# Kernel optimization log

Hardware: AMD Instinct MI355X
Metric: run time of the kernel (lower is better)

The kernel has to match this reference:

```python
import jax, jax.numpy as jnp
import numpy as np

TWO_PI = 2.0 * np.pi
OMEGA = 1.0  # frequency scale from init


def setup_inputs() -> dict:
    key = jax.random.key(0)
    ks = jax.random.split(key, 10)
    B, G, D = 2, 32, 3
    C_IN, C, C_OUT, F, L = 4, 128, 2, 128, 4  # in/model/out channels, freqs, n_spectral_convs
    a = jax.random.normal(ks[0], (B, G, G, G, C_IN), dtype=jnp.float32)
    x = jax.random.uniform(ks[1], (B, G, G, G, D), dtype=jnp.float32)
    y = jax.random.uniform(ks[2], (B, G, G, G, D), dtype=jnp.float32)
    fc_in_w = jax.random.normal(ks[3], (C_IN, C), dtype=jnp.float32) / np.sqrt(C_IN)
    fc_in_b = jnp.zeros((C,), dtype=jnp.float32)
    freqs = jax.random.normal(ks[4], (L, F, D), dtype=jnp.float32)  # per-layer spatial frequencies
    w_real = jax.random.normal(ks[5], (L, C, C, F), dtype=jnp.float32) * 0.05
    w_imag = jax.random.normal(ks[6], (L, C, C, F), dtype=jnp.float32) * 0.05
    fc_out_w = jax.random.normal(ks[7], (C, C_OUT), dtype=jnp.float32) / np.sqrt(C)
    fc_out_b = jnp.zeros((C_OUT,), dtype=jnp.float32)
    return {"a": a, "x": x, "y": y, "fc_in_w": fc_in_w, "fc_in_b": fc_in_b,
            "freqs": freqs, "w_real": w_real, "w_imag": w_imag,
            "fc_out_w": fc_out_w, "fc_out_b": fc_out_b}


def _spectral_conv(hf, xin, xout, k, Wc):
    # hf: (B, N, C) real; xin/xout: (B, N, D); k: (F, D); Wc: (C, C, F) complex
    N = hf.shape[1]
    ang_in = TWO_PI * OMEGA * jnp.einsum('bnd,fd->bnf', xin, k)
    phi_in = jnp.exp(-1j * ang_in.astype(jnp.complex64))          # (B, N, F)
    H = jnp.einsum('bnc,bnf->bcf', hf.astype(jnp.complex64), phi_in) / N  # forward transform
    G = jnp.einsum('bcf,cof->bof', H, Wc)                          # per-frequency channel mixing
    ang_out = TWO_PI * OMEGA * jnp.einsum('bnd,fd->bnf', xout, k)
    phi_out = jnp.exp(1j * ang_out.astype(jnp.complex64))          # (B, N, F)
    return jnp.real(jnp.einsum('bof,bnf->bno', G, phi_out))       # inverse evaluation at xout


def reference(a, x, y, fc_in_w, fc_in_b, freqs, w_real, w_imag, fc_out_w, fc_out_b):
    B = a.shape[0]
    spatial = a.shape[1:4]
    hf = jnp.einsum('...i,io->...o', a, fc_in_w) + fc_in_b
    hf = hf.reshape(B, -1, hf.shape[-1])               # (B, N, C)
    xf = x.reshape(B, -1, x.shape[-1])                 # (B, N, D)
    yf = y.reshape(B, -1, y.shape[-1])
    L = freqs.shape[0]
    for l in range(L):
        Wc = (w_real[l] + 1j * w_imag[l]).astype(jnp.complex64)
        pts_out = xf if l < L - 1 else yf              # last conv queries at y
        hf = jax.nn.gelu(_spectral_conv(hf, xf, pts_out, freqs[l], Wc))
    u = jnp.einsum('bnc,co->bno', hf, fc_out_w) + fc_out_b
    return u.reshape(B, *spatial, fc_out_w.shape[-1])
```

## Files before the change

### kernel.cpp

```cpp
#include <hip/hip_runtime.h>
#include <math.h>

#define Bb 2
#define Nn 32768
#define Cc 128
#define Ff 128
#define LL 4
#define SKN 128
#define PS 16448

typedef __attribute__((ext_vector_type(8))) short short8;
typedef __attribute__((ext_vector_type(4))) float float4v;
typedef __attribute__((ext_vector_type(2))) unsigned int uint2v;
typedef unsigned short ushort_t;
typedef unsigned int uint_t;

union frag_cast { short8 s; uint_t u[4]; };
union vec8 { float4v v[2]; float s[8]; };

__device__ inline uint_t asu(float f) { union { float f; uint_t u; } x; x.f = f; return x.u; }
__device__ inline float asf(uint_t u) { union { uint_t u; float f; } x; x.u = u; return x.f; }
__device__ inline uint_t pack_hi(float v0, float v1) {
    return __builtin_amdgcn_perm(asu(v1), asu(v0), 0x07060302u);
}
__device__ inline float resid(float v) { return v - asf(asu(v) & 0xffff0000u); }

typedef __attribute__((address_space(1))) const uint_t guint;
typedef __attribute__((address_space(3))) uint_t luint;
__device__ inline void gload16(const uint_t* g, uint_t* l) {
    __builtin_amdgcn_global_load_lds((guint*)g, (luint*)l, 16, 0, 0);
}

#define LBAR() asm volatile("s_waitcnt lgkmcnt(0)\n\ts_barrier" ::: "memory")
#define CBAR() asm volatile("s_waitcnt vmcnt(6) lgkmcnt(0)\n\ts_barrier" ::: "memory")

__global__ __launch_bounds__(256) void prep_xt(const float* __restrict__ x,
                                               const float* __restrict__ y,
                                               float* __restrict__ xT,
                                               float* __restrict__ yT) {
    int i = blockIdx.x * 256 + threadIdx.x;
    int b = i >> 15, n = i & 32767;
    const float* xp = x + (size_t)i * 3;
    const float* yp = y + (size_t)i * 3;
    size_t base = ((size_t)(b * 3) << 15) + n;
    xT[base] = xp[0]; xT[base + (1 << 15)] = xp[1]; xT[base + (2 << 15)] = xp[2];
    yT[base] = yp[0]; yT[base + (1 << 15)] = yp[1]; yT[base + (2 << 15)] = yp[2];
}

__global__ __launch_bounds__(256) void in_proj(const float* __restrict__ a,
                                               const float* __restrict__ w,
                                               const float* __restrict__ bias,
                                               uint_t* __restrict__ hfTh,
                                               uint_t* __restrict__ hfTl) {
    int idx = blockIdx.x * 256 + threadIdx.x;
    int np = idx & 16383;
    int c = (idx >> 14) & 127;
    int b = idx >> 21;
    int n = np * 2;
    const float* ap = a + (((size_t)(b << 15)) + n) * 4;
    float s0 = bias[c], s1 = s0;
#pragma unroll
    for (int i = 0; i < 4; ++i) { s0 += ap[i] * w[i * Cc + c]; s1 += ap[4 + i] * w[i * Cc + c]; }
    hfTh[idx] = pack_hi(s0, s1);
    hfTl[idx] = pack_hi(resid(s0), resid(s1));
}

__global__ __launch_bounds__(512, 2) void fwd_lds(const uint_t* __restrict__ hfTh,
                                                  const uint_t* __restrict__ hfTl,
                                                  const float* __restrict__ xT,
                                                  const float* __restrict__ freqs,
                                                  float* __restrict__ Spart) {
    __shared__ __align__(16) uint_t Ah_s[2][2048], Al_s[2][2048];

    const int sk = blockIdx.x;
    const int b = blockIdx.y;
    const int tid = threadIdx.x, lane = tid & 63, wave = tid >> 6;
    const int h = wave & 1, wn = wave >> 1;
    const int fr = lane & 15, kg = lane >> 4;

    float kx[2], ky[2], kz[2];
#pragma unroll
    for (int ni = 0; ni < 2; ++ni) {
        int f = wn * 32 + ni * 16 + fr;
        kx[ni] = freqs[f * 3 + 0];
        ky[ni] = freqs[f * 3 + 1];
        kz[ni] = freqs[f * 3 + 2];
    }

    const float* xb = xT + ((size_t)(b * 3) << 15);

    const int srow = wave * 16 + (lane >> 2);
    const size_t gbase = ((size_t)(b * 128 + srow) << 14) + (size_t)((lane & 3) * 4);
    const int npair0 = sk * 128;

    float4v acc[8][2];
#pragma unroll
    for (int mi = 0; mi < 8; ++mi)
#pragma unroll
        for (int ni = 0; ni < 2; ++ni) acc[mi][ni] = (float4v){0.f, 0.f, 0.f, 0.f};

    vec8 X0[2], X1[2], X2[2];
    gload16(hfTh + gbase + npair0, &Ah_s[0][wave * 256]);
    gload16(hfTl + gbase + npair0, &Al_s[0][wave * 256]);
    __builtin_amdgcn_sched_barrier(0);
    {
        const int nbase = sk * 256 + kg * 8;
        X0[0].v[0] = *(const float4v*)(xb + nbase);
        X0[0].v[1] = *(const float4v*)(xb + nbase + 4);
        X1[0].v[0] = *(const float4v*)(xb + (1 << 15) + nbase);
        X1[0].v[1] = *(const float4v*)(xb + (1 << 15) + nbase + 4);
        X2[0].v[0] = *(const float4v*)(xb + (2 << 15) + nbase);
        X2[0].v[1] = *(const float4v*)(xb + (2 << 15) + nbase + 4);
    }

#pragma unroll
    for (int kt = 0; kt < 8; ++kt) {
        const int cur = kt & 1, nxt = cur ^ 1;
        CBAR();
        if (kt < 7) {
            gload16(hfTh + gbase + npair0 + (kt + 1) * 16, &Ah_s[nxt][wave * 256]);
            gload16(hfTl + gbase + npair0 + (kt + 1) * 16, &Al_s[nxt][wave * 256]);
            __builtin_amdgcn_sched_barrier(0);
            const int nbase2 = sk * 256 + (kt + 1) * 32 + kg * 8;
            X0[nxt].v[0] = *(const float4v*)(xb + nbase2);
            X0[nxt].v[1] = *(const float4v*)(xb + nbase2 + 4);
            X1[nxt].v[0] = *(const float4v*)(xb + (1 << 15) + nbase2);
            X1[nxt].v[1] = *(const float4v*)(xb + (1 << 15) + nbase2 + 4);
            X2[nxt].v[0] = *(const float4v*)(xb + (2 << 15) + nbase2);
            X2[nxt].v[1] = *(const float4v*)(xb + (2 << 15) + nbase2 + 4);
        }
        float r[16], tv[16];
#pragma unroll
        for (int ni = 0; ni < 2; ++ni)
#pragma unroll
            for (int q = 0; q < 4; ++q) {
                float rv0 = X0[cur].s[2 * q] * kx[ni] + X1[cur].s[2 * q] * ky[ni] + X2[cur].s[2 * q] * kz[ni];
                float rv1 = X0[cur].s[2 * q + 1] * kx[ni] + X1[cur].s[2 * q + 1] * ky[ni] + X2[cur].s[2 * q + 1] * kz[ni];
                r[ni * 8 + 2 * q] = __builtin_amdgcn_fractf(rv0);
                r[ni * 8 + 2 * q + 1] = __builtin_amdgcn_fractf(rv1);
            }
        if (h) {
#pragma unroll
            for (int i = 0; i < 16; ++i) tv[i] = __builtin_amdgcn_sinf(r[i]);
        } else {
#pragma unroll
            for (int i = 0; i < 16; ++i) tv[i] = __builtin_amdgcn_cosf(r[i]);
        }
        frag_cast bhf[2], blf[2];
#pragma unroll
        for (int ni = 0; ni < 2; ++ni)
#pragma unroll
            for (int q = 0; q < 4; ++q) {
                float v0 = tv[ni * 8 + 2 * q], v1 = tv[ni * 8 + 2 * q + 1];
                bhf[ni].u[q] = pack_hi(v0, v1);
                blf[ni].u[q] = pack_hi(resid(v0), resid(v1));
            }
#pragma unroll
        for (int mi = 0; mi < 8; ++mi) {
            frag_cast ah, al;
            ah.s = *(const short8*)&Ah_s[cur][(mi * 16 + fr) * 16 + kg * 4];
            al.s = *(const short8*)&Al_s[cur][(mi * 16 + fr) * 16 + kg * 4];
#pragma unroll
            for (int ni = 0; ni < 2; ++ni) {
                acc[mi][ni] = __builtin_amdgcn_mfma_f32_16x16x32_bf16(ah.s, bhf[ni].s, acc[mi][ni], 0, 0, 0);
                acc[mi][ni] = __builtin_amdgcn_mfma_f32_16x16x32_bf16(ah.s, blf[ni].s, acc[mi][ni], 0, 0, 0);
                acc[mi][ni] = __builtin_amdgcn_mfma_f32_16x16x32_bf16(al.s, bhf[ni].s, acc[mi][ni], 0, 0, 0);
            }
        }
    }

    float* op = Spart + (size_t)((b * 2 + h) * SKN + sk) * PS;
#pragma unroll
    for (int mi = 0; mi < 8; ++mi)
#pragma unroll
        for (int ni = 0; ni < 2; ++ni)
#pragma unroll
            for (int r2 = 0; r2 < 4; ++r2) {
                int c = mi * 16 + kg * 4 + r2;
                int f = wn * 32 + ni * 16 + fr;
                op[c * 128 + f] = acc[mi][ni][r2];
            }
}

__global__ __launch_bounds__(256) void reduce_kernel(const float* __restrict__ Spart,
                                                     float* __restrict__ S) {
    __shared__ float red[4][64];
    const int chunk = blockIdx.x, bh = blockIdx.y;
    const int tid = threadIdx.x;
    const int cfl = tid & 63, q = tid >> 6;
    const float* p = Spart + (size_t)bh * SKN * PS + (size_t)(q * 32) * PS + chunk * 64 + cfl;
    float s = 0.0f;
#pragma unroll 8
    for (int k = 0; k < 32; ++k) s += p[(size_t)k * PS];
    red[q][cfl] = s;
    __syncthreads();
    if (tid < 64) {
        float t = red[0][tid] + red[1][tid] + red[2][tid] + red[3][tid];
        S[bh * 16384 + chunk * 64 + tid] = t;
    }
}

__global__ __launch_bounds__(256) void mix_kernel(const float* __restrict__ S,
                                                  const float* __restrict__ Wre,
                                                  const float* __restrict__ Wim,
                                                  uint_t* __restrict__ Gh,
                                                  uint_t* __restrict__ Gl) {
    __shared__ float Stile[4][128][16];
    const int ot = blockIdx.x;
    const int ft = blockIdx.y;
    const int tid = threadIdx.x;
    const int fl = tid & 15, ol = (tid >> 4) & 1, cg = tid >> 5;
    const int o = ot * 2 + ol, f0 = ft * 16;

    for (int i = tid; i < 8192; i += 256) {
        int bh = i >> 11, c = (i >> 4) & 127, ff = i & 15;
        Stile[bh][c][ff] = S[(size_t)bh * 16384 + c * 128 + f0 + ff];
    }
    __syncthreads();

    float g0 = 0.f, g1 = 0.f, g2 = 0.f, g3 = 0.f;
#pragma unroll 4
    for (int c = cg * 16; c < cg * 16 + 16; ++c) {
        float wr = Wre[((size_t)(c * 128 + o)) * 128 + f0 + fl];
        float wi = Wim[((size_t)(c * 128 + o)) * 128 + f0 + fl];
        float sc0 = Stile[0][c][fl], ss0 = Stile[1][c][fl];
        float sc1 = Stile[2][c][fl], ss1 = Stile[3][c][fl];
        g0 += sc0 * wr + ss0 * wi;  g1 += ss0 * wr - sc0 * wi;
        g2 += sc1 * wr + ss1 * wi;  g3 += ss1 * wr - sc1 * wi;
    }
    __syncthreads();
    float4v* rp = (float4v*)Stile;
    rp[cg * 32 + ol * 16 + fl] = (float4v){g0, g1, g2, g3};
    __syncthreads();
    if (tid < 32) {
        int tol = tid >> 4, tfl = tid & 15;
        float4v r = rp[tid];
#pragma unroll
        for (int j = 1; j < 8; ++j) r += rp[j * 32 + tid];
        const float invN = 1.0f / (float)Nn;
        float gre0 = r[0] * invN, gmi0 = r[1] * invN;
        float gre1 = r[2] * invN, gmi1 = r[3] * invN;
        int oo = ot * 2 + tol;
        Gh[(0 * 128 + oo) * 128 + f0 + tfl] = pack_hi(gre0, gmi0);
        Gl[(0 * 128 + oo) * 128 + f0 + tfl] = pack_hi(resid(gre0), resid(gmi0));
        Gh[(1 * 128 + oo) * 128 + f0 + tfl] = pack_hi(gre1, gmi1);
        Gl[(1 * 128 + oo) * 128 + f0 + tfl] = pack_hi(resid(gre1), resid(gmi1));
    }
}

template <int LAST>
__global__ __launch_bounds__(512, 4) void inv_reg(const uint_t* __restrict__ Gh,
                                                  const uint_t* __restrict__ Gl,
                                                  const float* __restrict__ ptsT,
                                                  const float* __restrict__ freqs,
                                                  uint_t* __restrict__ hfTh,
                                                  uint_t* __restrict__ hfTl,
                                                  const float* __restrict__ ow,
                                                  const float* __restrict__ ob,
                                                  float* __restrict__ u) {
    __shared__ __align__(16) float kxs[128], kys[128], kzs[128];
    __shared__ __align__(16) uint_t Ah_s[4096];
    __shared__ __align__(16) uint_t Al_s[4096];
    __shared__ float redo[8][32][2];
    const int nt = blockIdx.x, b = blockIdx.y;
    const int tid = threadIdx.x, lane = tid & 63, wn = tid >> 6;
    const int fr = lane & 15, kg = lane >> 4;

    if (tid < 128) {
        kxs[tid] = freqs[tid * 3 + 0];
        kys[tid] = freqs[tid * 3 + 1];
        kzs[tid] = freqs[tid * 3 + 2];
    }

    frag_cast bh[8], bl[8];
#pragma unroll
    for (int kt = 0; kt < 8; ++kt) {
        size_t gi = ((size_t)(b * 128 + wn * 16 + fr)) * 128 + kt * 16 + kg * 4;
        bh[kt].s = *(const short8*)(Gh + gi);
        bl[kt].s = *(const short8*)(Gl + gi);
    }

    float w0v = 0.f, w1v = 0.f;
    if (LAST) {
        int o = wn * 16 + fr;
        w0v = ow[o * 2 + 0];
        w1v = ow[o * 2 + 1];
    }

    const float* pb = ptsT + ((size_t)(b * 3) << 15);
    const int n0 = nt * 64;

    float px[4], py[4], pz[4];
#pragma unroll
    for (int m = 0; m < 4; ++m) {
        int n = n0 + m * 16 + fr;
        px[m] = pb[n]; py[m] = pb[(1 << 15) + n]; pz[m] = pb[(2 << 15) + n];
    }

    __syncthreads();

#pragma unroll
    for (int ph = 0; ph < 2; ++ph) {
        {
            const int kt = wn;
            float4v kxv = *(const float4v*)&kxs[kt * 16 + kg * 4];
            float4v kyv = *(const float4v*)&kys[kt * 16 + kg * 4];
            float4v kzv = *(const float4v*)&kzs[kt * 16 + kg * 4];
#pragma unroll
            for (int mi2 = 0; mi2 < 2; ++mi2) {
                const int m = ph * 2 + mi2;
                frag_cast ah, al;
#pragma unroll
                for (int q = 0; q < 4; ++q) {
                    float rev = px[m] * kxv[q] + py[m] * kyv[q] + pz[m] * kzv[q];
                    float rr = __builtin_amdgcn_fractf(rev);
                    float cv = __builtin_amdgcn_cosf(rr);
                    float sv = __builtin_amdgcn_sinf(rr);
                    ah.u[q] = pack_hi(cv, sv);
                    al.u[q] = pack_hi(resid(cv), resid(sv));
                }
                *(short8*)&Ah_s[((mi2 * 8 + kt) * 64 + lane) * 4] = ah.s;
                *(short8*)&Al_s[((mi2 * 8 + kt) * 64 + lane) * 4] = al.s;
            }
        }
        LBAR();

        float4v acc[2];
#pragma unroll
        for (int mi2 = 0; mi2 < 2; ++mi2) acc[mi2] = (float4v){0.f, 0.f, 0.f, 0.f};

#pragma unroll
        for (int kt = 0; kt < 8; ++kt) {
#pragma unroll
            for (int mi2 = 0; mi2 < 2; ++mi2) {
                frag_cast ah, al;
                ah.s = *(const short8*)&Ah_s[((mi2 * 8 + kt) * 64 + lane) * 4];
                al.s = *(const short8*)&Al_s[((mi2 * 8 + kt) * 64 + lane) * 4];
                acc[mi2] = __builtin_amdgcn_mfma_f32_16x16x32_bf16(ah.s, bh[kt].s, acc[mi2], 0, 0, 0);
                acc[mi2] = __builtin_amdgcn_mfma_f32_16x16x32_bf16(ah.s, bl[kt].s, acc[mi2], 0, 0, 0);
                acc[mi2] = __builtin_amdgcn_mfma_f32_16x16x32_bf16(al.s, bh[kt].s, acc[mi2], 0, 0, 0);
            }
        }
        LBAR();

        float ps[2][2][4];
        if (LAST) {
#pragma unroll
            for (int mi2 = 0; mi2 < 2; ++mi2)
#pragma unroll
                for (int j = 0; j < 2; ++j)
#pragma unroll
                    for (int r2 = 0; r2 < 4; ++r2) ps[mi2][j][r2] = 0.f;
        }
#pragma unroll
        for (int mi2 = 0; mi2 < 2; ++mi2) {
            const int m = ph * 2 + mi2;
            float g[4];
#pragma unroll
            for (int r2 = 0; r2 < 4; ++r2) {
                float v = acc[mi2][r2];
                float u2 = 1.5957691216057308f * (v + 0.044715f * v * v * v);
                float t = 1.0f - 2.0f / (1.0f + __expf(u2));
                g[r2] = 0.5f * v * (1.0f + t);
            }
            if (!LAST) {
                int o = wn * 16 + fr;
                int nb = n0 + m * 16 + kg * 4;
                size_t di = ((size_t)(b * 128 + o) << 14) + (nb >> 1);
                uint2v hv = { pack_hi(g[0], g[1]), pack_hi(g[2], g[3]) };
                uint2v lv = { pack_hi(resid(g[0]), resid(g[1])), pack_hi(resid(g[2]), resid(g[3])) };
                *(uint2v*)(hfTh + di) = hv;
                *(uint2v*)(hfTl + di) = lv;
            } else {
#pragma unroll
                for (int r2 = 0; r2 < 4; ++r2) {
                    ps[mi2][0][r2] += g[r2] * w0v;
                    ps[mi2][1][r2] += g[r2] * w1v;
                }
            }
        }

        if (LAST) {
#pragma unroll
            for (int mi2 = 0; mi2 < 2; ++mi2)
#pragma unroll
                for (int j = 0; j < 2; ++j)
#pragma unroll
                    for (int r2 = 0; r2 < 4; ++r2) {
                        float v = ps[mi2][j][r2];
                        v += __shfl_xor(v, 1);
                        v += __shfl_xor(v, 2);
                        v += __shfl_xor(v, 4);
                        v += __shfl_xor(v, 8);
                        ps[mi2][j][r2] = v;
                    }
            if (fr == 0) {
#pragma unroll
                for (int mi2 = 0; mi2 < 2; ++mi2)
#pragma unroll
                    for (int r2 = 0; r2 < 4; ++r2) {
                        redo[wn][mi2 * 16 + kg * 4 + r2][0] = ps[mi2][0][r2];
                        redo[wn][mi2 * 16 + kg * 4 + r2][1] = ps[mi2][1][r2];
                    }
            }
            LBAR();
            if (tid < 64) {
                int nl = tid >> 1, j = tid & 1;
                float val = ob[j];
#pragma unroll
                for (int w8 = 0; w8 < 8; ++w8) val += redo[w8][nl][j];
                u[((size_t)((b << 15) + n0 + ph * 32 + nl)) * 2 + j] = val;
            }
            LBAR();
        }
    }
}

extern "C" void kernel_launch(void* const* d_in, const int* in_sizes, int n_in,
                              void* d_out, int out_size, void* d_ws, size_t ws_size,
                              hipStream_t stream) {
    const float* a        = (const float*)d_in[0];
    const float* x        = (const float*)d_in[1];
    const float* y        = (const float*)d_in[2];
    const float* fc_in_w  = (const float*)d_in[3];
    const float* fc_in_b  = (const float*)d_in[4];
    const float* freqs    = (const float*)d_in[5];
    const float* w_real   = (const float*)d_in[6];
    const float* w_imag   = (const float*)d_in[7];
    const float* fc_out_w = (const float*)d_in[8];
    const float* fc_out_b = (const float*)d_in[9];
    float* out = (float*)d_out;

    uint_t* ws    = (uint_t*)d_ws;
    uint_t* hfTh  = ws;
    uint_t* hfTl  = hfTh + (size_t)Bb * Cc * Nn / 2;
    float*  Spart = (float*)(hfTl + (size_t)Bb * Cc * Nn / 2);
    float*  S     = Spart + (size_t)Bb * 2 * SKN * PS;
    uint_t* Gh    = (uint_t*)(S + (size_t)Bb * 2 * Cc * Ff);
    uint_t* Gl    = Gh + (size_t)Bb * Cc * Ff;
    float*  xT    = (float*)(Gl + (size_t)Bb * Cc * Ff);
    float*  yT    = xT + (size_t)Bb * 3 * Nn;

    prep_xt<<<(Bb * Nn) / 256, 256, 0, stream>>>(x, y, xT, yT);
    in_proj<<<(Bb * Cc * Nn / 2) / 256, 256, 0, stream>>>(a, fc_in_w, fc_in_b, hfTh, hfTl);

    for (int l = 0; l < LL; ++l) {
        const float* k   = freqs  + (size_t)l * Ff * 3;
        const float* Wre = w_real + (size_t)l * Cc * Cc * Ff;
        const float* Wim = w_imag + (size_t)l * Cc * Cc * Ff;
        const float* pT  = (l < LL - 1) ? xT : yT;

        fwd_lds<<<dim3(SKN, Bb), 512, 0, stream>>>(hfTh, hfTl, xT, k, Spart);
        reduce_kernel<<<dim3(256, 4), 256, 0, stream>>>(Spart, S);
        mix_kernel<<<dim3(64, 8), 256, 0, stream>>>(S, Wre, Wim, Gh, Gl);
        if (l < LL - 1) {
            inv_reg<0><<<dim3(512, Bb), 512, 0, stream>>>(Gh, Gl, pT, k, hfTh, hfTl,
                                                          nullptr, nullptr, nullptr);
        } else {
            inv_reg<1><<<dim3(512, Bb), 512, 0, stream>>>(Gh, Gl, pT, k, hfTh, hfTl,
                                                          fc_out_w, fc_out_b, out);
        }
    }
}
```

Baseline: 365.9 us.

## Fuse inverse evaluation, GELU and next layer's forward transform into one kernel

Adds an inv_fwd kernel that, per chunk of 256 points, evaluates the inverse transform from the mixed spectrum, applies GELU, and immediately accumulates the next layer's forward transform partial sums from LDS. The hidden activations hfTh/hfTl are no longer written to and re-read from global memory between layers, and one kernel launch per layer is removed. In exchange the fused kernel runs with a larger LDS footprint and register pressure (launch bound 512 threads, 2 blocks) and only 128x2 blocks, which may lower occupancy and parallelism compared with the separate kernels.

```diff
diff --git a/kernel.cpp b/kernel.cpp
--- a/kernel.cpp
+++ b/kernel.cpp
@@ -88,7 +88,6 @@
     }
 
     const float* xb = xT + ((size_t)(b * 3) << 15);
-
     const int srow = wave * 16 + (lane >> 2);
     const size_t gbase = ((size_t)(b * 128 + srow) << 14) + (size_t)((lane & 3) * 4);
     const int npair0 = sk * 128;
@@ -179,6 +178,184 @@
                 int c = mi * 16 + kg * 4 + r2;
                 int f = wn * 32 + ni * 16 + fr;
                 op[c * 128 + f] = acc[mi][ni][r2];
+            }
+}
+
+__global__ __launch_bounds__(512, 2) void inv_fwd(const uint_t* __restrict__ Gh,
+                                                  const uint_t* __restrict__ Gl,
+                                                  const float* __restrict__ xT,
+                                                  const float* __restrict__ fI,
+                                                  const float* __restrict__ fF,
+                                                  float* __restrict__ Spart) {
+    __shared__ float kxs[128], kys[128], kzs[128];
+    __shared__ __align__(16) float Xs[3][256];
+    __shared__ __align__(16) uint_t Ah_s[4096], Al_s[4096];
+    __shared__ __align__(16) uint_t Hh_s[2560], Hl_s[2560];
+    const int chunk = blockIdx.x, b = blockIdx.y;
+    const int tid = threadIdx.x, lane = tid & 63, wn = tid >> 6;
+    const int fr = lane & 15, kg = lane >> 4;
+    const int h = wn & 1, wf = wn >> 1;
+    const int n0 = chunk * 256;
+
+    if (tid < 128) {
+        kxs[tid] = fI[tid * 3 + 0];
+        kys[tid] = fI[tid * 3 + 1];
+        kzs[tid] = fI[tid * 3 + 2];
+    }
+    for (int i = tid; i < 768; i += 512) {
+        int d = i >> 8, nn = i & 255;
+        Xs[d][nn] = xT[((size_t)(b * 3 + d) << 15) + n0 + nn];
+    }
+
+    frag_cast bh[8], bl[8];
+#pragma unroll
+    for (int kt = 0; kt < 8; ++kt) {
+        size_t gi = ((size_t)(b * 128 + wn * 16 + fr)) * 128 + kt * 16 + kg * 4;
+        bh[kt].s = *(const short8*)(Gh + gi);
+        bl[kt].s = *(const short8*)(Gl + gi);
+    }
+
+    float kxf[2], kyf[2], kzf[2];
+#pragma unroll
+    for (int ni = 0; ni < 2; ++ni) {
+        int f = wf * 32 + ni * 16 + fr;
+        kxf[ni] = fF[f * 3 + 0];
+        kyf[ni] = fF[f * 3 + 1];
+        kzf[ni] = fF[f * 3 + 2];
+    }
+
+    float4v accF[8][2];
+#pragma unroll
+    for (int mi = 0; mi < 8; ++mi)
+#pragma unroll
+        for (int ni = 0; ni < 2; ++ni) accF[mi][ni] = (float4v){0.f, 0.f, 0.f, 0.f};
+
+    __syncthreads();
+
+    for (int p = 0; p < 8; ++p) {
+        const int nsub = p * 32;
+
+        {
+            const int kt = wn;
+            float4v kxv = *(const float4v*)&kxs[kt * 16 + kg * 4];
+            float4v kyv = *(const float4v*)&kys[kt * 16 + kg * 4];
+            float4v kzv = *(const float4v*)&kzs[kt * 16 + kg * 4];
+#pragma unroll
+            for (int mi2 = 0; mi2 < 2; ++mi2) {
+                float px = Xs[0][nsub + mi2 * 16 + fr];
+                float py = Xs[1][nsub + mi2 * 16 + fr];
+                float pz = Xs[2][nsub + mi2 * 16 + fr];
+                frag_cast ah, al;
+#pragma unroll
+                for (int q = 0; q < 4; ++q) {
+                    float rev = px * kxv[q] + py * kyv[q] + pz * kzv[q];
+                    float rr = __builtin_amdgcn_fractf(rev);
+                    float cv = __builtin_amdgcn_cosf(rr);
+                    float sv = __builtin_amdgcn_sinf(rr);
+                    ah.u[q] = pack_hi(cv, sv);
+                    al.u[q] = pack_hi(resid(cv), resid(sv));
+                }
+                *(short8*)&Ah_s[((mi2 * 8 + kt) * 64 + lane) * 4] = ah.s;
+                *(short8*)&Al_s[((mi2 * 8 + kt) * 64 + lane) * 4] = al.s;
+            }
+        }
+        LBAR();
+
+        {
+            float4v acc[2];
+#pragma unroll
+            for (int mi2 = 0; mi2 < 2; ++mi2) acc[mi2] = (float4v){0.f, 0.f, 0.f, 0.f};
+#pragma unroll
+            for (int kt = 0; kt < 8; ++kt) {
+#pragma unroll
+                for (int mi2 = 0; mi2 < 2; ++mi2) {
+                    frag_cast ah, al;
+                    ah.s = *(const short8*)&Ah_s[((mi2 * 8 + kt) * 64 + lane) * 4];
+                    al.s = *(const short8*)&Al_s[((mi2 * 8 + kt) * 64 + lane) * 4];
+                    acc[mi2] = __builtin_amdgcn_mfma_f32_16x16x32_bf16(ah.s, bh[kt].s, acc[mi2], 0, 0, 0);
+                    acc[mi2] = __builtin_amdgcn_mfma_f32_16x16x32_bf16(ah.s, bl[kt].s, acc[mi2], 0, 0, 0);
+                    acc[mi2] = __builtin_amdgcn_mfma_f32_16x16x32_bf16(al.s, bh[kt].s, acc[mi2], 0, 0, 0);
+                }
+            }
+#pragma unroll
+            for (int mi2 = 0; mi2 < 2; ++mi2) {
+                float g[4];
+#pragma unroll
+                for (int r2 = 0; r2 < 4; ++r2) {
+                    float v = acc[mi2][r2];
+                    float u2 = 1.5957691216057308f * (v + 0.044715f * v * v * v);
+                    float t = 1.0f - 2.0f / (1.0f + __expf(u2));
+                    g[r2] = 0.5f * v * (1.0f + t);
+                }
+                int row = wn * 16 + fr;
+                uint2v hv = { pack_hi(g[0], g[1]), pack_hi(g[2], g[3]) };
+                uint2v lv = { pack_hi(resid(g[0]), resid(g[1])), pack_hi(resid(g[2]), resid(g[3])) };
+                *(uint2v*)&Hh_s[row * 20 + mi2 * 8 + kg * 2] = hv;
+                *(uint2v*)&Hl_s[row * 20 + mi2 * 8 + kg * 2] = lv;
+            }
+        }
+        LBAR();
+
+        {
+            vec8 x0, x1, x2;
+            x0.v[0] = *(const float4v*)&Xs[0][nsub + kg * 8];
+            x0.v[1] = *(const float4v*)&Xs[0][nsub + kg * 8 + 4];
+            x1.v[0] = *(const float4v*)&Xs[1][nsub + kg * 8];
+            x1.v[1] = *(const float4v*)&Xs[1][nsub + kg * 8 + 4];
+            x2.v[0] = *(const float4v*)&Xs[2][nsub + kg * 8];
+            x2.v[1] = *(const float4v*)&Xs[2][nsub + kg * 8 + 4];
+            float r[16], tv[16];
+#pragma unroll
+            for (int ni = 0; ni < 2; ++ni)
+#pragma unroll
+                for (int q = 0; q < 4; ++q) {
+                    float rv0 = x0.s[2 * q] * kxf[ni] + x1.s[2 * q] * kyf[ni] + x2.s[2 * q] * kzf[ni];
+                    float rv1 = x0.s[2 * q + 1] * kxf[ni] + x1.s[2 * q + 1] * kyf[ni] + x2.s[2 * q + 1] * kzf[ni];
+                    r[ni * 8 + 2 * q] = __builtin_amdgcn_fractf(rv0);
+                    r[ni * 8 + 2 * q + 1] = __builtin_amdgcn_fractf(rv1);
+                }
+            if (h) {
+#pragma unroll
+                for (int i = 0; i < 16; ++i) tv[i] = __builtin_amdgcn_sinf(r[i]);
+            } else {
+#pragma unroll
+                for (int i = 0; i < 16; ++i) tv[i] = __builtin_amdgcn_cosf(r[i]);
+            }
+            frag_cast bhf[2], blf[2];
+#pragma unroll
+            for (int ni = 0; ni < 2; ++ni)
+#pragma unroll
+                for (int q = 0; q < 4; ++q) {
+                    float v0 = tv[ni * 8 + 2 * q], v1 = tv[ni * 8 + 2 * q + 1];
+                    bhf[ni].u[q] = pack_hi(v0, v1);
+                    blf[ni].u[q] = pack_hi(resid(v0), resid(v1));
+                }
+#pragma unroll
+            for (int mi = 0; mi < 8; ++mi) {
+                frag_cast ah, al;
+                ah.s = *(const short8*)&Hh_s[(mi * 16 + fr) * 20 + kg * 4];
+                al.s = *(const short8*)&Hl_s[(mi * 16 + fr) * 20 + kg * 4];
+#pragma unroll
+                for (int ni = 0; ni < 2; ++ni) {
+                    accF[mi][ni] = __builtin_amdgcn_mfma_f32_16x16x32_bf16(ah.s, bhf[ni].s, accF[mi][ni], 0, 0, 0);
+                    accF[mi][ni] = __builtin_amdgcn_mfma_f32_16x16x32_bf16(ah.s, blf[ni].s, accF[mi][ni], 0, 0, 0);
+                    accF[mi][ni] = __builtin_amdgcn_mfma_f32_16x16x32_bf16(al.s, bhf[ni].s, accF[mi][ni], 0, 0, 0);
+                }
+            }
+        }
+        LBAR();
+    }
+
+    float* op = Spart + (size_t)((b * 2 + h) * SKN + chunk) * PS;
+#pragma unroll
+    for (int mi = 0; mi < 8; ++mi)
+#pragma unroll
+        for (int ni = 0; ni < 2; ++ni)
+#pragma unroll
+            for (int r2 = 0; r2 < 4; ++r2) {
+                int c = mi * 16 + kg * 4 + r2;
+                int f = wf * 32 + ni * 16 + fr;
+                op[c * 128 + f] = accF[mi][ni][r2];
             }
 }
 
@@ -328,7 +505,6 @@
         float4v acc[2];
 #pragma unroll
         for (int mi2 = 0; mi2 < 2; ++mi2) acc[mi2] = (float4v){0.f, 0.f, 0.f, 0.f};
-
 #pragma unroll
         for (int kt = 0; kt < 8; ++kt) {
 #pragma unroll
@@ -444,21 +620,21 @@
     prep_xt<<<(Bb * Nn) / 256, 256, 0, stream>>>(x, y, xT, yT);
     in_proj<<<(Bb * Cc * Nn / 2) / 256, 256, 0, stream>>>(a, fc_in_w, fc_in_b, hfTh, hfTl);
 
-    for (int l = 0; l < LL; ++l) {
-        const float* k   = freqs  + (size_t)l * Ff * 3;
-        const float* Wre = w_real + (size_t)l * Cc * Cc * Ff;
-        const float* Wim = w_imag + (size_t)l * Cc * Cc * Ff;
-        const float* pT  = (l < LL - 1) ? xT : yT;
-
-        fwd_lds<<<dim3(SKN, Bb), 512, 0, stream>>>(hfTh, hfTl, xT, k, Spart);
+    fwd_lds<<<dim3(SKN, Bb), 512, 0, stream>>>(hfTh, hfTl, xT, freqs, Spart);
+    reduce_kernel<<<dim3(256, 4), 256, 0, stream>>>(Spart, S);
+    mix_kernel<<<dim3(64, 8), 256, 0, stream>>>(S, w_real, w_imag, Gh, Gl);
+
+    for (int l = 0; l < LL - 1; ++l) {
+        const float* kI  = freqs  + (size_t)l * Ff * 3;
+        const float* kF  = freqs  + (size_t)(l + 1) * Ff * 3;
+        const float* Wre = w_real + (size_t)(l + 1) * Cc * Cc * Ff;
+        const float* Wim = w_imag + (size_t)(l + 1) * Cc * Cc * Ff;
+
+        inv_fwd<<<dim3(128, Bb), 512, 0, stream>>>(Gh, Gl, xT, kI, kF, Spart);
         reduce_kernel<<<dim3(256, 4), 256, 0, stream>>>(Spart, S);
         mix_kernel<<<dim3(64, 8), 256, 0, stream>>>(S, Wre, Wim, Gh, Gl);
-        if (l < LL - 1) {
-            inv_reg<0><<<dim3(512, Bb), 512, 0, stream>>>(Gh, Gl, pT, k, hfTh, hfTl,
-                                                          nullptr, nullptr, nullptr);
-        } else {
-            inv_reg<1><<<dim3(512, Bb), 512, 0, stream>>>(Gh, Gl, pT, k, hfTh, hfTl,
-                                                          fc_out_w, fc_out_b, out);
-        }
-    }
-}
+    }
+
+    inv_reg<1><<<dim3(512, Bb), 512, 0, stream>>>(Gh, Gl, yT, freqs + (size_t)(LL - 1) * Ff * 3,
+                                                  hfTh, hfTl, fc_out_w, fc_out_b, out);
+}
```

After: 330.8 us. 9.6% less time.
